# Kernel optimization log

Measured on AMD Instinct MI355X. Metric: run time of the kernel, lower is better.

## Reference

```python
import jax, jax.numpy as jnp
import numpy as np

DICT = 32768
TOP_K = 128
LN_EPS = 1e-5


def setup_inputs() -> dict:
    key = jax.random.key(0)
    k_x, k_we, k_be, k_wd, k_bd = jax.random.split(key, 5)
    B, S, D = 4, 2048, 768
    x = jax.random.normal(k_x, (B, S, D), dtype=jnp.float32)
    # nn.Linear stores weight as [out, in]; init scaled roughly like orthogonal gains
    W_enc = jax.random.normal(k_we, (DICT, D), dtype=jnp.float32) / np.sqrt(D)
    b_enc = jax.random.normal(k_be, (DICT,), dtype=jnp.float32) * 0.01
    W_dec = jax.random.normal(k_wd, (D, DICT), dtype=jnp.float32) * (0.1 / np.sqrt(DICT))
    b_dec = jax.random.normal(k_bd, (D,), dtype=jnp.float32) * 0.01
    ln_gamma = jnp.ones((DICT,), dtype=jnp.float32)
    ln_beta = jnp.zeros((DICT,), dtype=jnp.float32)
    return {"x": x, "W_enc": W_enc, "b_enc": b_enc, "ln_gamma": ln_gamma,
            "ln_beta": ln_beta, "W_dec": W_dec, "b_dec": b_dec}


def _layernorm(z, gamma, beta):
    mu = jnp.mean(z, axis=-1, keepdims=True)
    var = jnp.mean(jnp.square(z - mu), axis=-1, keepdims=True)
    return (z - mu) * jax.lax.rsqrt(var + LN_EPS) * gamma + beta


def _top_k_activation(z, k):
    # keep top-k values per row, zero elsewhere (scatter, like torch.scatter_)
    vals, idx = jax.lax.top_k(z, k)            # [B,S,k]
    out = jnp.zeros_like(z)
    return jnp.put_along_axis(out, idx, vals, axis=-1, inplace=False)


def reference(x, W_enc, b_enc, ln_gamma, ln_beta, W_dec, b_dec):
    # encoder: [B,S,D] @ [D,DICT] -> [B,S,DICT]
    z = jnp.einsum("bsd,fd->bsf", x, W_enc) + b_enc
    z = _layernorm(z, ln_gamma, ln_beta)
    z = jax.nn.relu(z)
    features = _top_k_activation(z, TOP_K)      # [B,S,DICT], mostly zero
    output = jnp.einsum("bsf,df->bsd", features, W_dec) + b_dec  # [B,S,D]
    return (output, features)
```

## Files before the change

### kernel.cpp

```cpp
#include <hip/hip_runtime.h>
#include <hip/hip_bf16.h>

#define R_TOT  8192
#define DIM    768
#define FDICT  32768
#define TOPK   128
#define LN_EPS 1e-5f
#define BAND_M 0.12f
#define BAND_CAP 192

using f32x4  = __attribute__((ext_vector_type(4))) float;
using short8 = __attribute__((ext_vector_type(8))) short;

__device__ inline short f2bf(float f) {
    __hip_bfloat16 h = __float2bfloat16(f);
    return *reinterpret_cast<short*>(&h);
}
__device__ inline float bf2f(short s) {
    return __uint_as_float(((unsigned)(unsigned short)s) << 16);
}
__device__ inline void load_lds16(const void* g, void* l) {
    __builtin_amdgcn_global_load_lds(
        (const __attribute__((address_space(1))) unsigned int*)g,
        (__attribute__((address_space(3))) unsigned int*)l, 16, 0, 0);
}

__global__ __launch_bounds__(256) void conv_bf16(
    const float* __restrict__ in, unsigned short* __restrict__ out, int n8)
{
    const int i0 = blockIdx.x * 256 + threadIdx.x;
    const int stride = gridDim.x * 256;
    for (int g = i0; g < n8; g += stride) {
        const float4 a = ((const float4*)in)[g * 2];
        const float4 b = ((const float4*)in)[g * 2 + 1];
        short8 v;
        v[0] = f2bf(a.x); v[1] = f2bf(a.y); v[2] = f2bf(a.z); v[3] = f2bf(a.w);
        v[4] = f2bf(b.x); v[5] = f2bf(b.y); v[6] = f2bf(b.z); v[7] = f2bf(b.w);
        ((short8*)out)[g] = v;
    }
}

__global__ __launch_bounds__(256) void prep_gb(
    const float* __restrict__ gamma, const float* __restrict__ beta,
    float* __restrict__ gbinfo)
{
    __shared__ float rr[16];
    const int t = threadIdx.x;
    const int w = t >> 6;
    float gmn = 1e30f, gmx = -1e30f, bmn = 1e30f, bmx = -1e30f;
    for (int i = t; i < FDICT / 4; i += 256) {
        const float4 g4 = ((const float4*)gamma)[i];
        const float4 b4 = ((const float4*)beta)[i];
        gmn = fminf(gmn, fminf(fminf(g4.x, g4.y), fminf(g4.z, g4.w)));
        gmx = fmaxf(gmx, fmaxf(fmaxf(g4.x, g4.y), fmaxf(g4.z, g4.w)));
        bmn = fminf(bmn, fminf(fminf(b4.x, b4.y), fminf(b4.z, b4.w)));
        bmx = fmaxf(bmx, fmaxf(fmaxf(b4.x, b4.y), fmaxf(b4.z, b4.w)));
    }
#pragma unroll
    for (int o = 32; o > 0; o >>= 1) {
        gmn = fminf(gmn, __shfl_down(gmn, o, 64));
        gmx = fmaxf(gmx, __shfl_down(gmx, o, 64));
        bmn = fminf(bmn, __shfl_down(bmn, o, 64));
        bmx = fmaxf(bmx, __shfl_down(bmx, o, 64));
    }
    if ((t & 63) == 0) {
        rr[w * 4 + 0] = gmn; rr[w * 4 + 1] = gmx;
        rr[w * 4 + 2] = bmn; rr[w * 4 + 3] = bmx;
    }
    __syncthreads();
    if (t == 0) {
        float a = rr[0], b = rr[1], c = rr[2], d = rr[3];
        for (int i = 1; i < 4; ++i) {
            a = fminf(a, rr[i * 4 + 0]); b = fmaxf(b, rr[i * 4 + 1]);
            c = fminf(c, rr[i * 4 + 2]); d = fmaxf(d, rr[i * 4 + 3]);
        }
        gbinfo[0] = fmaxf(fabsf(a), fabsf(b));
        gbinfo[1] = fmaxf(fabsf(c), fabsf(d));
        gbinfo[2] = (a == b && c == d) ? 1.f : 0.f;
        gbinfo[3] = b;
        gbinfo[4] = d;
    }
}

#define READ_A(P)                                                              \
    af00 = *(const short8*)&Sb[abase + (2*(P))*1024 + sw0];                    \
    af01 = *(const short8*)&Sb[abase + (2*(P))*1024 + sw1];                    \
    af10 = *(const short8*)&Sb[abase + (2*(P)+1)*1024 + sw0];                  \
    af11 = *(const short8*)&Sb[abase + (2*(P)+1)*1024 + sw1];

#define DO_MFMA(P)                                                             \
    __builtin_amdgcn_s_setprio(1);                                             \
    _Pragma("unroll")                                                          \
    for (int n = 0; n < 4; ++n) {                                              \
        acc[2*(P)][n]   = __builtin_amdgcn_mfma_f32_16x16x32_bf16(af00, bf0[n], acc[2*(P)][n],   0,0,0); \
        acc[2*(P)][n]   = __builtin_amdgcn_mfma_f32_16x16x32_bf16(af01, bf1[n], acc[2*(P)][n],   0,0,0); \
        acc[2*(P)+1][n] = __builtin_amdgcn_mfma_f32_16x16x32_bf16(af10, bf0[n], acc[2*(P)+1][n], 0,0,0); \
        acc[2*(P)+1][n] = __builtin_amdgcn_mfma_f32_16x16x32_bf16(af11, bf1[n], acc[2*(P)+1][n], 0,0,0); \
    }                                                                          \
    __builtin_amdgcn_s_setprio(0);

__global__ __launch_bounds__(512, 2) void enc_gemm(
    const unsigned short* __restrict__ Xb, const unsigned short* __restrict__ Wb,
    const float* __restrict__ benc, unsigned short* __restrict__ Zb)
{
    __shared__ __align__(16) unsigned short S[65536];

    const int t = threadIdx.x;
    const int w = t >> 6, l = t & 63;

    const int cpx = (int)gridDim.x >> 3;
    const int swz = ((int)blockIdx.x & 7) * cpx + ((int)blockIdx.x >> 3);
    const long bm = (long)(swz >> 7) * 256;
    const long bn = (long)(swz & 127) * 256;

    const int wm = w >> 2, wn = w & 3;
    const int lrow = l & 15, l4 = l >> 4;

    const int sw0 = ((l4     ) ^ (lrow & 7)) * 8;
    const int sw1 = ((4 + l4 ) ^ (lrow & 7)) * 8;
    const int abase = wm * 8192 + lrow * 64;
    const int bbase = 16384 + wn * 4096 + lrow * 64;

    const int rh0 = w * 16 + (l >> 3);
    const int rh1 = rh0 + 8;
    const int gsl = ((l & 7) ^ (l >> 3)) * 8;
    const unsigned short* pA00 = Xb + (bm +       rh0) * DIM + gsl;
    const unsigned short* pA01 = Xb + (bm +       rh1) * DIM + gsl;
    const unsigned short* pA10 = Xb + (bm + 128 + rh0) * DIM + gsl;
    const unsigned short* pA11 = Xb + (bm + 128 + rh1) * DIM + gsl;
    const unsigned short* pB00 = Wb + (bn +       rh0) * DIM + gsl;
    const unsigned short* pB01 = Wb + (bn +       rh1) * DIM + gsl;
    const unsigned short* pB10 = Wb + (bn + 128 + rh0) * DIM + gsl;
    const unsigned short* pB11 = Wb + (bn + 128 + rh1) * DIM + gsl;
    const int d00 = w * 1024;
    const int d01 = w * 1024 + 512;

    f32x4 acc[8][4];
#pragma unroll
    for (int m = 0; m < 8; ++m)
#pragma unroll
        for (int n = 0; n < 4; ++n) acc[m][n] = (f32x4){0.f, 0.f, 0.f, 0.f};

    load_lds16(pA00, S + d00);
    load_lds16(pA01, S + d01);
    load_lds16(pA10, S + 8192 + d00);
    load_lds16(pA11, S + 8192 + d01);
    load_lds16(pB00, S + 16384 + d00);
    load_lds16(pB01, S + 16384 + d01);
    load_lds16(pB10, S + 16384 + 8192 + d00);
    load_lds16(pB11, S + 16384 + 8192 + d01);
    pA00 += 64; pA01 += 64; pA10 += 64; pA11 += 64;
    pB00 += 64; pB01 += 64; pB10 += 64; pB11 += 64;

    short8 bf0[4], bf1[4];
    short8 af00, af01, af10, af11;

#pragma unroll 1
    for (int kt = 0; kt < 12; ++kt) {
        const unsigned short* Sb = S + (kt & 1) * 32768;
        unsigned short*       Sn = S + ((kt & 1) ^ 1) * 32768;

        if (kt < 11) {
            load_lds16(pA00, Sn + d00);
            load_lds16(pA01, Sn + d01);
            load_lds16(pA10, Sn + 8192 + d00);
            load_lds16(pA11, Sn + 8192 + d01);
            asm volatile("s_waitcnt vmcnt(4)" ::: "memory");
        } else {
            asm volatile("s_waitcnt vmcnt(0)" ::: "memory");
        }
        __builtin_amdgcn_s_barrier();
#pragma unroll
        for (int n = 0; n < 4; ++n) {
            bf0[n] = *(const short8*)&Sb[bbase + n * 1024 + sw0];
            bf1[n] = *(const short8*)&Sb[bbase + n * 1024 + sw1];
        }
        READ_A(0)
        DO_MFMA(0)
        asm volatile("" ::: "memory");
        __builtin_amdgcn_s_barrier();

        READ_A(1)
        if (kt < 11) {
            load_lds16(pB00, Sn + 16384 + d00);
            load_lds16(pB01, Sn + 16384 + d01);
            load_lds16(pB10, Sn + 16384 + 8192 + d00);
            load_lds16(pB11, Sn + 16384 + 8192 + d01);
        }
        asm volatile("" ::: "memory");
        __builtin_amdgcn_s_barrier();
        DO_MFMA(1)
        asm volatile("" ::: "memory");
        __builtin_amdgcn_s_barrier();

        READ_A(2)
        asm volatile("" ::: "memory");
        __builtin_amdgcn_s_barrier();
        DO_MFMA(2)
        asm volatile("" ::: "memory");
        __builtin_amdgcn_s_barrier();

        READ_A(3)
        asm volatile("" ::: "memory");
        __builtin_amdgcn_s_barrier();
        DO_MFMA(3)
        asm volatile("" ::: "memory");
        __builtin_amdgcn_s_barrier();

        pA00 += 64; pA01 += 64; pA10 += 64; pA11 += 64;
        pB00 += 64; pB01 += 64; pB10 += 64; pB11 += 64;
    }

    __syncthreads();
    float bias[4];
#pragma unroll
    for (int n = 0; n < 4; ++n) bias[n] = benc[bn + wn * 64 + n * 16 + lrow];
    unsigned short* Cs = S;
#pragma unroll
    for (int m = 0; m < 8; ++m)
#pragma unroll
        for (int n = 0; n < 4; ++n)
#pragma unroll
            for (int q = 0; q < 4; ++q)
                Cs[(wm * 128 + m * 16 + l4 * 4 + q) * 256 + wn * 64 + n * 16 + lrow] =
                    (unsigned short)f2bf(acc[m][n][q] + bias[n]);
    __syncthreads();
#pragma unroll
    for (int it = 0; it < 16; ++it) {
        const int g = t + it * 512;
        const int row = g >> 5;
        const int c8 = (g & 31) * 8;
        const short8 v = *(const short8*)&Cs[row * 256 + c8];
        __builtin_nontemporal_store(v, (short8*)&Zb[(bm + row) * FDICT + bn + c8]);
    }
}

__global__ __launch_bounds__(1024) void topk_select(
    const unsigned short* __restrict__ Zb, const float* __restrict__ gamma,
    const float* __restrict__ beta, const float* __restrict__ gbinfo,
    int* __restrict__ sel_idx, float* __restrict__ sel_val,
    int* __restrict__ band_idx, int* __restrict__ cdef, int* __restrict__ nband,
    float* __restrict__ muarr, float* __restrict__ sinvarr,
    float* __restrict__ feat)
{
    __shared__ float    redf[32];
    __shared__ unsigned cacc[16];
    __shared__ unsigned scomp[2];

    const int t = threadIdx.x;
    const int w = t >> 6;
    const long r = blockIdx.x;

    if (t < 16) cacc[t] = 0u;
    if (t == 16) { scomp[0] = 0u; scomp[1] = 0u; }

    unsigned u[32];
    float sum = 0.f, sumsq = 0.f;
    const short8* Z8 = (const short8*)(Zb + r * (size_t)FDICT);
#pragma unroll
    for (int q = 0; q < 4; ++q) {
        const short8 v = Z8[q * 1024 + t];
#pragma unroll
        for (int j = 0; j < 8; ++j) {
            const float f = bf2f(v[j]);
            u[q * 8 + j] = __float_as_uint(f);
            sum += f; sumsq += f * f;
        }
    }
#pragma unroll
    for (int o = 32; o > 0; o >>= 1) {
        sum   += __shfl_down(sum, o, 64);
        sumsq += __shfl_down(sumsq, o, 64);
    }
    if ((t & 63) == 0) { redf[w] = sum; redf[16 + w] = sumsq; }
    __syncthreads();
    float s_ = 0.f, sq_ = 0.f;
#pragma unroll
    for (int i = 0; i < 16; ++i) { s_ += redf[i]; sq_ += redf[16 + i]; }
    const float mu = s_ / (float)FDICT;
    float var = sq_ / (float)FDICT - mu * mu;
    if (var < 0.f) var = 0.f;
    const float sinv = 1.f / sqrtf(var + LN_EPS);

    const float g0 = gbinfo[3], b0 = gbinfo[4];
    const bool uniform = (gbinfo[2] != 0.f) && (g0 > 0.f) && (g0 <= 2.f);

    if (uniform) {
        const float gs = sinv * g0;
#pragma unroll
        for (int i = 0; i < 32; ++i)
            u[i] = __float_as_uint(fmaxf(
                fmaf(__uint_as_float(u[i]) - mu, gs, b0), 0.f));
    } else {
#pragma unroll
        for (int q = 0; q < 4; ++q) {
            const size_t base = (size_t)(q * 1024 + t) * 8;
            const float4 g4a = *(const float4*)(gamma + base);
            const float4 g4b = *(const float4*)(gamma + base + 4);
            const float4 b4a = *(const float4*)(beta + base);
            const float4 b4b = *(const float4*)(beta + base + 4);
            const float gs[8] = {g4a.x, g4a.y, g4a.z, g4a.w, g4b.x, g4b.y, g4b.z, g4b.w};
            const float bs[8] = {b4a.x, b4a.y, b4a.z, b4a.w, b4b.x, b4b.y, b4b.z, b4b.w};
#pragma unroll
            for (int j = 0; j < 8; ++j) {
                const int i = q * 8 + j;
                u[i] = __float_as_uint(fmaxf(
                    fmaf((__uint_as_float(u[i]) - mu) * sinv, gs[j], bs[j]), 0.f));
            }
        }
    }

    float Tf = 0.f;
    bool got = false;
    int nextacc = 0;
    if (uniform) {
        const float Vh = fmaf(2.6601f, g0, b0);
        const float h  = 0.25f * g0;
        float lo = Vh - h, hi = Vh + h;
        unsigned pc = 0;
#pragma unroll
        for (int i = 0; i < 32; ++i) {
            const float a = __uint_as_float(u[i]);
            pc += (a > lo) ? 1u : 0u;
            pc += (a > hi) ? 0x10000u : 0u;
        }
#pragma unroll
        for (int o = 32; o > 0; o >>= 1) pc += __shfl_down(pc, o, 64);
        if ((t & 63) == 0) atomicAdd(&cacc[0], pc);
        __syncthreads();
        const unsigned clo = cacc[0] & 0xFFFFu, chi = cacc[0] >> 16;
        if (clo >= TOPK && chi < TOPK) {
#pragma unroll 1
            for (int it = 1; it <= 3; ++it) {
                const float thr = 0.5f * (lo + hi);
                unsigned cnt = 0;
#pragma unroll
                for (int i = 0; i < 32; ++i)
                    cnt += (__uint_as_float(u[i]) > thr) ? 1u : 0u;
#pragma unroll
                for (int o = 32; o > 0; o >>= 1) cnt += __shfl_down(cnt, o, 64);
                if ((t & 63) == 0) atomicAdd(&cacc[it], cnt);
                __syncthreads();
                if (cacc[it] >= TOPK) lo = thr; else hi = thr;
            }
            Tf = 0.5f * (lo + hi);
            got = true;
        }
        nextacc = 4;
    }
    if (!got) {
        __syncthreads();
        float vmax = 0.f;
#pragma unroll
        for (int i = 0; i < 32; ++i) vmax = fmaxf(vmax, __uint_as_float(u[i]));
#pragma unroll
        for (int o = 32; o > 0; o >>= 1) vmax = fmaxf(vmax, __shfl_down(vmax, o, 64));
        if ((t & 63) == 0) redf[w] = vmax;
        __syncthreads();
        float mx = 0.f;
#pragma unroll
        for (int i = 0; i < 16; ++i) mx = fmaxf(mx, redf[i]);
        float lo = 0.f, hi = mx + 1e-6f;
#pragma unroll 1
        for (int it = 0; it < 12; ++it) {
            const float thr = 0.5f * (lo + hi);
            unsigned cnt = 0;
#pragma unroll
            for (int i = 0; i < 32; ++i)
                cnt += (__uint_as_float(u[i]) > thr) ? 1u : 0u;
#pragma unroll
            for (int o = 32; o > 0; o >>= 1) cnt += __shfl_down(cnt, o, 64);
            if ((t & 63) == 0) atomicAdd(&cacc[nextacc + it], cnt);
            __syncthreads();
            if (cacc[nextacc + it] >= TOPK) lo = thr; else hi = thr;
        }
        Tf = 0.5f * (lo + hi);
    }

    const float thi = Tf + BAND_M, tlo = Tf - BAND_M;

#pragma unroll
    for (int i = 0; i < 32; ++i) {
        const float a = __uint_as_float(u[i]);
        const int idx = ((i >> 3) * 1024 + t) * 8 + (i & 7);
        if (a > thi) {
            const unsigned s2 = atomicAdd(&scomp[0], 1u);
            sel_idx[r * TOPK + s2] = idx;
            sel_val[r * TOPK + s2] = a;
        } else if (a >= tlo) {
            const unsigned s2 = atomicAdd(&scomp[1], 1u);
            if (s2 < BAND_CAP) band_idx[r * BAND_CAP + s2] = idx;
        }
    }
    __syncthreads();
    if (t == 0) {
        cdef[r]  = (int)scomp[0];
        int nb = (int)scomp[1]; if (nb > BAND_CAP) nb = BAND_CAP;
        nband[r] = nb;
        muarr[r] = mu; sinvarr[r] = sinv;
    }
    if (feat) {
        const f32x4 z4 = (f32x4){0.f, 0.f, 0.f, 0.f};
        f32x4* row4 = (f32x4*)(feat + r * (size_t)FDICT);
#pragma unroll
        for (int q = 0; q < 8; ++q)
            __builtin_nontemporal_store(z4, &row4[q * 1024 + t]);
    }
}

__global__ __launch_bounds__(256) void refine_select(
    const float* __restrict__ X, const float* __restrict__ Wenc,
    const float* __restrict__ benc, const float* __restrict__ gamma,
    const float* __restrict__ beta, const int* __restrict__ band_idx,
    const int* __restrict__ cdef, const int* __restrict__ nband,
    const float* __restrict__ muarr, const float* __restrict__ sinvarr,
    int* __restrict__ sel_idx, float* __restrict__ sel_val,
    float* __restrict__ feat)
{
    __shared__ float xs[DIM];
    __shared__ float cval[BAND_CAP];
    __shared__ int   cidx[BAND_CAP];
    __shared__ int   scnt;
    const int t = threadIdx.x;
    const long r = blockIdx.x;
    const int w = t >> 6, l = t & 63;

    for (int i = t; i < DIM; i += 256) xs[i] = X[r * DIM + i];
    if (t == 0) scnt = 0;
    const int nb = nband[r];
    const int cd = cdef[r];
    int need = TOPK - cd; if (need > nb) need = nb;
    const double mu = (double)muarr[r], sinv = (double)sinvarr[r];

    if (feat && t < cd)
        feat[r * (size_t)FDICT + sel_idx[r * TOPK + t]] = sel_val[r * TOPK + t];
    __syncthreads();

    for (int c = w; c < nb; c += 4) {
        const int fi = band_idx[r * BAND_CAP + c];
        const float* wr = Wenc + (size_t)fi * DIM;
        double s = 0.0;
        for (int k = l; k < DIM; k += 64) s = fma((double)xs[k], (double)wr[k], s);
#pragma unroll
        for (int o = 32; o > 0; o >>= 1) s += __shfl_down(s, o, 64);
        if (l == 0) {
            const double z = s + (double)benc[fi];
            const double a = (z - mu) * sinv * (double)gamma[fi] + (double)beta[fi];
            cval[c] = fmaxf((float)a, 0.f);
            cidx[c] = fi;
        }
    }
    __syncthreads();
    if (t < nb) {
        const float v = cval[t];
        const int id = cidx[t];
        int rank = 0;
        for (int j = 0; j < nb; ++j) {
            const float vj = cval[j];
            rank += (vj > v) || (vj == v && cidx[j] < id);
        }
        if (rank < need) {
            const int s = atomicAdd(&scnt, 1);
            sel_idx[r * TOPK + cd + s] = id;
            sel_val[r * TOPK + cd + s] = v;
            if (feat) feat[r * (size_t)FDICT + id] = v;
        }
    }
}

__global__ __launch_bounds__(256) void transposeWd(
    const float* __restrict__ Wd, unsigned short* __restrict__ WdTb)
{
    __shared__ float tile[32][33];
    const int fx = blockIdx.x * 32;
    const int dy = blockIdx.y * 32;
    const int tx = threadIdx.x & 31;
    const int ty = threadIdx.x >> 5;
    for (int i = ty; i < 32; i += 8)
        tile[i][tx] = Wd[(size_t)(dy + i) * FDICT + fx + tx];
    __syncthreads();
    for (int i = ty; i < 32; i += 8)
        WdTb[(size_t)(fx + i) * DIM + dy + tx] = (unsigned short)f2bf(tile[tx][i]);
}

__global__ __launch_bounds__(384) void decode(
    const int* __restrict__ sel_idx, const float* __restrict__ sel_val,
    const unsigned short* __restrict__ WdTb, const float* __restrict__ bdec,
    float* __restrict__ out)
{
    __shared__ int   sidx[TOPK];
    __shared__ float sval[TOPK];
    const int t = threadIdx.x;
    const long r = blockIdx.x;
    if (t < TOPK) { sidx[t] = sel_idx[r * TOPK + t]; sval[t] = sel_val[r * TOPK + t]; }
    __syncthreads();
    const float2 b2 = *(const float2*)(bdec + t * 2);
    float a0 = b2.x, a1 = b2.y;
    for (int j = 0; j < TOPK; ++j) {
        const unsigned wp = *(const unsigned*)(WdTb + (size_t)sidx[j] * DIM + t * 2);
        const float v = sval[j];
        a0 = fmaf(v, __uint_as_float((wp & 0xFFFFu) << 16), a0);
        a1 = fmaf(v, __uint_as_float(wp & 0xFFFF0000u), a1);
    }
    float2 o2; o2.x = a0; o2.y = a1;
    *(float2*)(out + r * DIM + t * 2) = o2;
}

__global__ __launch_bounds__(1024) void featfill(
    const int* __restrict__ sel_idx, const float* __restrict__ sel_val,
    float* __restrict__ feat)
{
    const int t = threadIdx.x;
    const long r = blockIdx.x;
    const f32x4 z4 = (f32x4){0.f, 0.f, 0.f, 0.f};
    f32x4* row4 = (f32x4*)(feat + r * FDICT);
    for (int i = t; i < FDICT / 4; i += 1024)
        __builtin_nontemporal_store(z4, &row4[i]);
    __syncthreads();
    if (t < TOPK)
        feat[r * FDICT + sel_idx[r * TOPK + t]] = sel_val[r * TOPK + t];
}

extern "C" void kernel_launch(void* const* d_in, const int* in_sizes, int n_in,
                              void* d_out, int out_size, void* d_ws, size_t ws_size,
                              hipStream_t stream)
{
    const float* x     = (const float*)d_in[0];
    const float* Wenc  = (const float*)d_in[1];
    const float* benc  = (const float*)d_in[2];
    const float* gamma = (const float*)d_in[3];
    const float* beta  = (const float*)d_in[4];
    const float* Wdec  = (const float*)d_in[5];
    const float* bdec  = (const float*)d_in[6];

    float* out  = (float*)d_out;
    float* feat = out + (size_t)R_TOT * DIM;

    unsigned short* Xb = (unsigned short*)out;

    char* ws = (char*)d_ws;
    int*   sidx  = (int*)ws;
    float* sval  = (float*)(ws + (size_t)R_TOT * TOPK * 4);
    int*   bidx  = (int*)(ws + (size_t)R_TOT * TOPK * 8);
    int*   cdef  = (int*)(ws + (size_t)R_TOT * (TOPK * 8 + BAND_CAP * 4));
    int*   nbnd  = cdef + R_TOT;
    float* muarr = (float*)(nbnd + R_TOT);
    float* sinva = muarr + R_TOT;
    float* gbinfo = sinva + R_TOT;

    const size_t WS_NEED = 624ull << 20;
    const bool big = (ws_size >= WS_NEED);

    unsigned short* Zb, *Wb, *WdTb;
    if (big) {
        Zb   = (unsigned short*)(ws + (16ull << 20));
        Wb   = (unsigned short*)(ws + (528ull << 20));
        WdTb = (unsigned short*)(ws + (576ull << 20));
    } else {
        Zb   = (unsigned short*)feat;
        Wb   = (unsigned short*)((char*)feat + 536870912ull);
        WdTb = (unsigned short*)((char*)feat + 587202560ull);
    }
    float* featArg = big ? feat : nullptr;

    prep_gb<<<1, 256, 0, stream>>>(gamma, beta, gbinfo);
    conv_bf16<<<1536, 256, 0, stream>>>(x,    Xb, R_TOT * DIM / 8);
    conv_bf16<<<2048, 256, 0, stream>>>(Wenc, Wb, FDICT * DIM / 8);
    enc_gemm<<<4096, 512, 0, stream>>>(Xb, Wb, benc, Zb);
    topk_select<<<R_TOT, 1024, 0, stream>>>(Zb, gamma, beta, gbinfo,
                                            sidx, sval, bidx, cdef, nbnd,
                                            muarr, sinva, featArg);
    refine_select<<<R_TOT, 256, 0, stream>>>(x, Wenc, benc, gamma, beta,
                                             bidx, cdef, nbnd, muarr, sinva,
                                             sidx, sval, featArg);
    transposeWd<<<dim3(FDICT / 32, DIM / 32), 256, 0, stream>>>(Wdec, WdTb);
    decode<<<R_TOT, 384, 0, stream>>>(sidx, sval, WdTb, bdec, out);
    if (!big)
        featfill<<<R_TOT, 1024, 0, stream>>>(sidx, sval, feat);
}
```

Baseline: 1.790 ms.

## Fuse prep kernels into one launch, merge refine with decode, remap GEMM tiles

Merges the x/W_enc bf16 conversions, the W_dec transpose and the gamma/beta range scan into a single prep launch, with the work type chosen by block index. Fuses refine_select and decode into one 384-thread kernel that keeps the selected indices and values in LDS, so decode no longer re-reads them from global memory. Also changes the enc_gemm block-to-tile mapping so consecutive swizzled blocks walk the M tiles first, which changes L2 reuse of the weight tiles. Costs: the fused prep kernel has a heterogeneous grid, and refine_decode does the refine step with a wider block whose extra warps add little to that phase.

```diff
diff --git a/kernel.cpp b/kernel.cpp
--- a/kernel.cpp
+++ b/kernel.cpp
@@ -25,60 +25,84 @@
         (__attribute__((address_space(3))) unsigned int*)l, 16, 0, 0);
 }
 
-__global__ __launch_bounds__(256) void conv_bf16(
-    const float* __restrict__ in, unsigned short* __restrict__ out, int n8)
-{
-    const int i0 = blockIdx.x * 256 + threadIdx.x;
-    const int stride = gridDim.x * 256;
-    for (int g = i0; g < n8; g += stride) {
-        const float4 a = ((const float4*)in)[g * 2];
-        const float4 b = ((const float4*)in)[g * 2 + 1];
-        short8 v;
-        v[0] = f2bf(a.x); v[1] = f2bf(a.y); v[2] = f2bf(a.z); v[3] = f2bf(a.w);
-        v[4] = f2bf(b.x); v[5] = f2bf(b.y); v[6] = f2bf(b.z); v[7] = f2bf(b.w);
-        ((short8*)out)[g] = v;
-    }
-}
-
-__global__ __launch_bounds__(256) void prep_gb(
-    const float* __restrict__ gamma, const float* __restrict__ beta,
+__global__ __launch_bounds__(256) void prep_fused(
+    const float* __restrict__ x, const float* __restrict__ Wenc,
+    const float* __restrict__ Wdec, const float* __restrict__ gamma,
+    const float* __restrict__ beta, unsigned short* __restrict__ Xb,
+    unsigned short* __restrict__ Wb, unsigned short* __restrict__ WdTb,
     float* __restrict__ gbinfo)
 {
-    __shared__ float rr[16];
+    __shared__ float tile[32][33];
+    const int b = blockIdx.x;
     const int t = threadIdx.x;
-    const int w = t >> 6;
-    float gmn = 1e30f, gmx = -1e30f, bmn = 1e30f, bmx = -1e30f;
-    for (int i = t; i < FDICT / 4; i += 256) {
-        const float4 g4 = ((const float4*)gamma)[i];
-        const float4 b4 = ((const float4*)beta)[i];
-        gmn = fminf(gmn, fminf(fminf(g4.x, g4.y), fminf(g4.z, g4.w)));
-        gmx = fmaxf(gmx, fmaxf(fmaxf(g4.x, g4.y), fmaxf(g4.z, g4.w)));
-        bmn = fminf(bmn, fminf(fminf(b4.x, b4.y), fminf(b4.z, b4.w)));
-        bmx = fmaxf(bmx, fmaxf(fmaxf(b4.x, b4.y), fmaxf(b4.z, b4.w)));
-    }
-#pragma unroll
-    for (int o = 32; o > 0; o >>= 1) {
-        gmn = fminf(gmn, __shfl_down(gmn, o, 64));
-        gmx = fmaxf(gmx, __shfl_down(gmx, o, 64));
-        bmn = fminf(bmn, __shfl_down(bmn, o, 64));
-        bmx = fmaxf(bmx, __shfl_down(bmx, o, 64));
-    }
-    if ((t & 63) == 0) {
-        rr[w * 4 + 0] = gmn; rr[w * 4 + 1] = gmx;
-        rr[w * 4 + 2] = bmn; rr[w * 4 + 3] = bmx;
-    }
-    __syncthreads();
-    if (t == 0) {
-        float a = rr[0], b = rr[1], c = rr[2], d = rr[3];
-        for (int i = 1; i < 4; ++i) {
-            a = fminf(a, rr[i * 4 + 0]); b = fmaxf(b, rr[i * 4 + 1]);
-            c = fminf(c, rr[i * 4 + 2]); d = fmaxf(d, rr[i * 4 + 3]);
-        }
-        gbinfo[0] = fmaxf(fabsf(a), fabsf(b));
-        gbinfo[1] = fmaxf(fabsf(c), fabsf(d));
-        gbinfo[2] = (a == b && c == d) ? 1.f : 0.f;
-        gbinfo[3] = b;
-        gbinfo[4] = d;
+
+    if (b < 1536) {
+        const int n8 = R_TOT * DIM / 8;
+        for (int g = b * 256 + t; g < n8; g += 1536 * 256) {
+            const float4 a = ((const float4*)x)[g * 2];
+            const float4 c = ((const float4*)x)[g * 2 + 1];
+            short8 v;
+            v[0] = f2bf(a.x); v[1] = f2bf(a.y); v[2] = f2bf(a.z); v[3] = f2bf(a.w);
+            v[4] = f2bf(c.x); v[5] = f2bf(c.y); v[6] = f2bf(c.z); v[7] = f2bf(c.w);
+            ((short8*)Xb)[g] = v;
+        }
+    } else if (b < 3584) {
+        const int n8 = FDICT * DIM / 8;
+        for (int g = (b - 1536) * 256 + t; g < n8; g += 2048 * 256) {
+            const float4 a = ((const float4*)Wenc)[g * 2];
+            const float4 c = ((const float4*)Wenc)[g * 2 + 1];
+            short8 v;
+            v[0] = f2bf(a.x); v[1] = f2bf(a.y); v[2] = f2bf(a.z); v[3] = f2bf(a.w);
+            v[4] = f2bf(c.x); v[5] = f2bf(c.y); v[6] = f2bf(c.z); v[7] = f2bf(c.w);
+            ((short8*)Wb)[g] = v;
+        }
+    } else if (b < 3584 + 24576) {
+        const int b2 = b - 3584;
+        const int fx = (b2 & 1023) * 32;
+        const int dy = (b2 >> 10) * 32;
+        const int tx = t & 31;
+        const int ty = t >> 5;
+        for (int i = ty; i < 32; i += 8)
+            tile[i][tx] = Wdec[(size_t)(dy + i) * FDICT + fx + tx];
+        __syncthreads();
+        for (int i = ty; i < 32; i += 8)
+            WdTb[(size_t)(fx + i) * DIM + dy + tx] = (unsigned short)f2bf(tile[tx][i]);
+    } else {
+        float* rr = &tile[0][0];
+        const int w = t >> 6;
+        float gmn = 1e30f, gmx = -1e30f, bmn = 1e30f, bmx = -1e30f;
+        for (int i = t; i < FDICT / 4; i += 256) {
+            const float4 g4 = ((const float4*)gamma)[i];
+            const float4 b4 = ((const float4*)beta)[i];
+            gmn = fminf(gmn, fminf(fminf(g4.x, g4.y), fminf(g4.z, g4.w)));
+            gmx = fmaxf(gmx, fmaxf(fmaxf(g4.x, g4.y), fmaxf(g4.z, g4.w)));
+            bmn = fminf(bmn, fminf(fminf(b4.x, b4.y), fminf(b4.z, b4.w)));
+            bmx = fmaxf(bmx, fmaxf(fmaxf(b4.x, b4.y), fmaxf(b4.z, b4.w)));
+        }
+#pragma unroll
+        for (int o = 32; o > 0; o >>= 1) {
+            gmn = fminf(gmn, __shfl_down(gmn, o, 64));
+            gmx = fmaxf(gmx, __shfl_down(gmx, o, 64));
+            bmn = fminf(bmn, __shfl_down(bmn, o, 64));
+            bmx = fmaxf(bmx, __shfl_down(bmx, o, 64));
+        }
+        if ((t & 63) == 0) {
+            rr[w * 4 + 0] = gmn; rr[w * 4 + 1] = gmx;
+            rr[w * 4 + 2] = bmn; rr[w * 4 + 3] = bmx;
+        }
+        __syncthreads();
+        if (t == 0) {
+            float a = rr[0], b_ = rr[1], c = rr[2], d = rr[3];
+            for (int i = 1; i < 4; ++i) {
+                a = fminf(a, rr[i * 4 + 0]); b_ = fmaxf(b_, rr[i * 4 + 1]);
+                c = fminf(c, rr[i * 4 + 2]); d = fmaxf(d, rr[i * 4 + 3]);
+            }
+            gbinfo[0] = fmaxf(fabsf(a), fabsf(b_));
+            gbinfo[1] = fmaxf(fabsf(c), fabsf(d));
+            gbinfo[2] = (a == b_ && c == d) ? 1.f : 0.f;
+            gbinfo[3] = b_;
+            gbinfo[4] = d;
+        }
     }
 }
 
@@ -110,8 +134,8 @@
 
     const int cpx = (int)gridDim.x >> 3;
     const int swz = ((int)blockIdx.x & 7) * cpx + ((int)blockIdx.x >> 3);
-    const long bm = (long)(swz >> 7) * 256;
-    const long bn = (long)(swz & 127) * 256;
+    const long bm = (long)(swz & 31) * 256;
+    const long bn = (long)(swz >> 5) * 256;
 
     const int wm = w >> 2, wn = w & 3;
     const int lrow = l & 15, l4 = l >> 4;
@@ -408,35 +432,42 @@
     }
 }
 
-__global__ __launch_bounds__(256) void refine_select(
+__global__ __launch_bounds__(384) void refine_decode(
     const float* __restrict__ X, const float* __restrict__ Wenc,
     const float* __restrict__ benc, const float* __restrict__ gamma,
     const float* __restrict__ beta, const int* __restrict__ band_idx,
     const int* __restrict__ cdef, const int* __restrict__ nband,
     const float* __restrict__ muarr, const float* __restrict__ sinvarr,
     int* __restrict__ sel_idx, float* __restrict__ sel_val,
-    float* __restrict__ feat)
+    const unsigned short* __restrict__ WdTb, const float* __restrict__ bdec,
+    float* __restrict__ out, float* __restrict__ feat)
 {
     __shared__ float xs[DIM];
     __shared__ float cval[BAND_CAP];
     __shared__ int   cidx[BAND_CAP];
+    __shared__ int   sh_idx[TOPK];
+    __shared__ float sh_val[TOPK];
     __shared__ int   scnt;
     const int t = threadIdx.x;
     const long r = blockIdx.x;
     const int w = t >> 6, l = t & 63;
 
-    for (int i = t; i < DIM; i += 256) xs[i] = X[r * DIM + i];
+    for (int i = t; i < DIM; i += 384) xs[i] = X[r * DIM + i];
     if (t == 0) scnt = 0;
+    if (t < TOPK) { sh_idx[t] = 0; sh_val[t] = 0.f; }
     const int nb = nband[r];
     const int cd = cdef[r];
     int need = TOPK - cd; if (need > nb) need = nb;
     const double mu = (double)muarr[r], sinv = (double)sinvarr[r];
 
-    if (feat && t < cd)
-        feat[r * (size_t)FDICT + sel_idx[r * TOPK + t]] = sel_val[r * TOPK + t];
-    __syncthreads();
-
-    for (int c = w; c < nb; c += 4) {
+    if (t < cd) {
+        sh_idx[t] = sel_idx[r * TOPK + t];
+        sh_val[t] = sel_val[r * TOPK + t];
+        if (feat) feat[r * (size_t)FDICT + sh_idx[t]] = sh_val[t];
+    }
+    __syncthreads();
+
+    for (int c = w; c < nb; c += 6) {
         const int fi = band_idx[r * BAND_CAP + c];
         const float* wr = Wenc + (size_t)fi * DIM;
         double s = 0.0;
@@ -461,44 +492,21 @@
         }
         if (rank < need) {
             const int s = atomicAdd(&scnt, 1);
+            sh_idx[cd + s] = id;
+            sh_val[cd + s] = v;
             sel_idx[r * TOPK + cd + s] = id;
             sel_val[r * TOPK + cd + s] = v;
             if (feat) feat[r * (size_t)FDICT + id] = v;
         }
     }
-}
-
-__global__ __launch_bounds__(256) void transposeWd(
-    const float* __restrict__ Wd, unsigned short* __restrict__ WdTb)
-{
-    __shared__ float tile[32][33];
-    const int fx = blockIdx.x * 32;
-    const int dy = blockIdx.y * 32;
-    const int tx = threadIdx.x & 31;
-    const int ty = threadIdx.x >> 5;
-    for (int i = ty; i < 32; i += 8)
-        tile[i][tx] = Wd[(size_t)(dy + i) * FDICT + fx + tx];
-    __syncthreads();
-    for (int i = ty; i < 32; i += 8)
-        WdTb[(size_t)(fx + i) * DIM + dy + tx] = (unsigned short)f2bf(tile[tx][i]);
-}
-
-__global__ __launch_bounds__(384) void decode(
-    const int* __restrict__ sel_idx, const float* __restrict__ sel_val,
-    const unsigned short* __restrict__ WdTb, const float* __restrict__ bdec,
-    float* __restrict__ out)
-{
-    __shared__ int   sidx[TOPK];
-    __shared__ float sval[TOPK];
-    const int t = threadIdx.x;
-    const long r = blockIdx.x;
-    if (t < TOPK) { sidx[t] = sel_idx[r * TOPK + t]; sval[t] = sel_val[r * TOPK + t]; }
-    __syncthreads();
+    __syncthreads();
+
     const float2 b2 = *(const float2*)(bdec + t * 2);
     float a0 = b2.x, a1 = b2.y;
+#pragma unroll 1
     for (int j = 0; j < TOPK; ++j) {
-        const unsigned wp = *(const unsigned*)(WdTb + (size_t)sidx[j] * DIM + t * 2);
-        const float v = sval[j];
+        const unsigned wp = *(const unsigned*)(WdTb + (size_t)sh_idx[j] * DIM + t * 2);
+        const float v = sh_val[j];
         a0 = fmaf(v, __uint_as_float((wp & 0xFFFFu) << 16), a0);
         a1 = fmaf(v, __uint_as_float(wp & 0xFFFF0000u), a1);
     }
@@ -563,18 +571,15 @@
     }
     float* featArg = big ? feat : nullptr;
 
-    prep_gb<<<1, 256, 0, stream>>>(gamma, beta, gbinfo);
-    conv_bf16<<<1536, 256, 0, stream>>>(x,    Xb, R_TOT * DIM / 8);
-    conv_bf16<<<2048, 256, 0, stream>>>(Wenc, Wb, FDICT * DIM / 8);
+    prep_fused<<<1536 + 2048 + 24576 + 1, 256, 0, stream>>>(
+        x, Wenc, Wdec, gamma, beta, Xb, Wb, WdTb, gbinfo);
     enc_gemm<<<4096, 512, 0, stream>>>(Xb, Wb, benc, Zb);
     topk_select<<<R_TOT, 1024, 0, stream>>>(Zb, gamma, beta, gbinfo,
                                             sidx, sval, bidx, cdef, nbnd,
                                             muarr, sinva, featArg);
-    refine_select<<<R_TOT, 256, 0, stream>>>(x, Wenc, benc, gamma, beta,
+    refine_decode<<<R_TOT, 384, 0, stream>>>(x, Wenc, benc, gamma, beta,
                                              bidx, cdef, nbnd, muarr, sinva,
-                                             sidx, sval, featArg);
-    transposeWd<<<dim3(FDICT / 32, DIM / 32), 256, 0, stream>>>(Wdec, WdTb);
-    decode<<<R_TOT, 384, 0, stream>>>(sidx, sval, WdTb, bdec, out);
+                                             sidx, sval, WdTb, bdec, out, featArg);
     if (!big)
         featfill<<<R_TOT, 1024, 0, stream>>>(sidx, sval, feat);
 }
```

Measured after the change: 2.182 ms. 1.22x slower.
